# Kernel optimization log

Hardware: AMD Instinct MI355X
Metric: run time of the kernel (lower is better)

## Reference

```python
import jax, jax.numpy as jnp
import numpy as np

B, S, F, H = 2, 2048, 1024, 16
HD = F // H  # head_dim = 64


def rope_embedding(length: int, features: int) -> jnp.ndarray:
    # Faithful copy of the module's unusual RoPE: emb = concat[sin, cos] used as an
    # elementwise multiplier, with symmetric averaging for positions > 0.
    base = 10000.0
    inv_freq = 1.0 / base ** (jnp.arange(0, features, 2, dtype=jnp.float32) / features)
    sinusoid = jnp.einsum('i,j->ij', jnp.arange(length, dtype=jnp.float32), inv_freq)
    sin = jnp.sin(sinusoid)
    cos = jnp.cos(sinusoid)  # features even, so no trailing-column drop
    emb = jnp.concatenate([sin, cos], axis=1)[:, None, :]  # [L, 1, HD]
    if length > 1:
        emb_sym = (emb[1:] + emb[1:][::-1]) / 2.0
        emb = jnp.concatenate([emb[:1], emb_sym], axis=0)
    return emb


def setup_inputs() -> dict:
    key = jax.random.key(0)
    ks = jax.random.split(key, 6)
    scale = 1.0 / np.sqrt(F)
    kv = jax.random.normal(ks[0], (B, S, F), dtype=jnp.float32)
    q = jax.random.normal(ks[1], (B, S, F), dtype=jnp.float32)
    Wq = jax.random.normal(ks[2], (F, F), dtype=jnp.float32) * scale
    Wk = jax.random.normal(ks[3], (F, F), dtype=jnp.float32) * scale
    Wv = jax.random.normal(ks[4], (F, F), dtype=jnp.float32) * scale
    Wo = jax.random.normal(ks[5], (F, F), dtype=jnp.float32) * scale
    mask = jnp.tril(jnp.ones((S, S), dtype=bool))[None, None]  # causal [1,1,S,S]
    return {"kv": kv, "q": q, "Wq": Wq, "Wk": Wk, "Wv": Wv, "Wo": Wo, "mask": mask}


def reference(kv, q, Wq, Wk, Wv, Wo, mask):
    # Dense projections (use_bias=False)
    query = (q @ Wq).reshape(B, S, H, HD)
    key_ = (kv @ Wk).reshape(B, S, H, HD)
    value = (kv @ Wv).reshape(B, S, H, HD)
    # Inline RoPE multiply (module's variant)
    emb = rope_embedding(S, HD)  # [S, 1, HD]
    query = query * emb
    key_ = key_ * emb
    # Scores [B, H, Sq, Sk], scale, mask, softmax
    aw = jnp.einsum('bqhd,bkhd->bhqk', query, key_) / jnp.sqrt(jnp.float32(HD))
    aw = jnp.where(mask, aw, jnp.finfo(jnp.float32).min)
    aw = jax.nn.softmax(aw, axis=-1)
    out = jnp.einsum('bhqk,bkhd->bqhd', aw, value).reshape(B, S, F)
    return out @ Wo
```

## Files before the change

### kernel.cpp

```cpp
#include <hip/hip_runtime.h>

typedef unsigned short u16;
typedef unsigned int u32;

#define S_LEN 2048
#define FEAT 1024
#define NHEAD 16
#define HDIM 64
#define NBATCH 2
#define NROWS (NBATCH * S_LEN)

typedef float f32x4 __attribute__((ext_vector_type(4)));
typedef short s16x8 __attribute__((ext_vector_type(8)));
typedef u32 u32x2 __attribute__((ext_vector_type(2)));

#define LOG2E 1.4426950408889634f

__device__ inline u16 f2bf(float f) {
  u32 u = __float_as_uint(f);
  return (u16)((u + 0x7fffu + ((u >> 16) & 1u)) >> 16);
}

__device__ inline u32 cvt_pk_bf16(float lo, float hi) {
  u32 r;
  asm("v_cvt_pk_bf16_f32 %0, %1, %2" : "=v"(r) : "v"(lo), "v"(hi));
  return r;
}

__device__ inline float fexp2(float x) { return __builtin_amdgcn_exp2f(x); }

__device__ inline f32x4 mfma16(s16x8 a, s16x8 b, f32x4 c) {
  return __builtin_amdgcn_mfma_f32_16x16x32_bf16(a, b, c, 0, 0, 0);
}

typedef __attribute__((address_space(1))) void gvoid;
typedef __attribute__((address_space(3))) void lvoid;
__device__ inline void gload_lds16(const void* g, void* l) {
  __builtin_amdgcn_global_load_lds((gvoid*)g, (lvoid*)l, 16, 0, 0);
}

__device__ inline int swz64(int p) { return p ^ (((p >> 7) & 7) << 4); }

struct us4 { u16 x, y, z, w; };
__global__ __launch_bounds__(256) void prep_kernel(
    const float* __restrict__ q, const float* __restrict__ kv,
    const float* __restrict__ Wq, const float* __restrict__ Wk,
    const float* __restrict__ Wv, const float* __restrict__ Wo,
    u16* __restrict__ qbf, u16* __restrict__ kvbf,
    u16* __restrict__ WqT, u16* __restrict__ WkT,
    u16* __restrict__ WvT, u16* __restrict__ WoT,
    float* __restrict__ emb) {
  __shared__ float tile[32][33];
  int bid = blockIdx.x, tid = threadIdx.x;
  const int n4each = NROWS * FEAT / 4;
  if (bid < 8192) {
    int i = bid * 256 + tid;
    const float* in = q;
    u16* out = qbf;
    if (i >= n4each) { i -= n4each; in = kv; out = kvbf; }
    float4 v = ((const float4*)in)[i];
    us4 o;
    o.x = f2bf(v.x); o.y = f2bf(v.y); o.z = f2bf(v.z); o.w = f2bf(v.w);
    ((us4*)out)[i] = o;
  } else if (bid < 12288) {
    int idx = bid - 8192;
    int z = idx >> 10, rem = idx & 1023;
    int by = rem >> 5, bx = rem & 31;
    const float* W = z == 0 ? Wq : z == 1 ? Wk : z == 2 ? Wv : Wo;
    u16* O = z == 0 ? WqT : z == 1 ? WkT : z == 2 ? WvT : WoT;
    int tx = tid & 31, ty = tid >> 5;
    int bi = bx * 32, bo = by * 32;
#pragma unroll
    for (int r = 0; r < 32; r += 8) tile[ty + r][tx] = W[(bi + ty + r) * FEAT + bo + tx];
    __syncthreads();
#pragma unroll
    for (int r = 0; r < 32; r += 8) O[(bo + ty + r) * FEAT + bi + tx] = f2bf(tile[tx][ty + r]);
  } else {
    int i = (bid - 12288) * 256 + tid;
    if (i >= S_LEN * HDIM) return;
    int p = i >> 6, d = i & 63, j = d & 31;
    float invf = exp2f(-13.287712379549449f * (float)j / 32.0f);
    float a1 = (float)p * invf;
    float v1 = (d < 32) ? sinf(a1) : cosf(a1);
    float e;
    if (p == 0) {
      e = v1;
    } else {
      float a2 = (float)(S_LEN - p) * invf;
      float v2 = (d < 32) ? sinf(a2) : cosf(a2);
      e = 0.5f * (v1 + v2);
    }
    emb[i] = e;
  }
}

__global__ __launch_bounds__(256, 3) void gemm_qkv(
    const u16* __restrict__ qbf, const u16* __restrict__ kvbf,
    const u16* __restrict__ WqT, const u16* __restrict__ WkT, const u16* __restrict__ WvT,
    u16* __restrict__ Qb, u16* __restrict__ Kx, u16* __restrict__ Vx,
    const float* __restrict__ emb) {
  __shared__ __align__(16) u16 lA[3][128 * 32];
  __shared__ __align__(16) u16 lB[3][128 * 32];
  const int K = FEAT;
  int t = threadIdx.x;
  int w = t >> 6, l = t & 63;
  int lr = l & 15, lk = l >> 4;
  int flat = blockIdx.y * 32 + blockIdx.x;
  int xcd = flat & 7, idx = flat >> 3;
  int cx = xcd & 3, cy = xcd >> 2;
  int bx = cx * 8 + (idx & 7);
  int yy = cy * 12 + (idx >> 3);
  int mode = yy >> 3;
  int row0 = bx * 128, col0 = (yy & 7) * 128;
  int wm = w >> 1, wn = w & 1;

  const u16* A = mode == 0 ? qbf : kvbf;
  const u16* Bt = mode == 0 ? WqT : mode == 1 ? WkT : WvT;
  u16* Out = mode == 0 ? Qb : mode == 1 ? Kx : Vx;

  f32x4 acc[4][4] = {};

  int P0 = t * 16, P1 = P0 + 4096;
  int L0 = swz64(P0), L1 = swz64(P1);
  const char* Ab = (const char*)A;
  const char* Bb = (const char*)Bt;
  size_t aOff0 = (size_t)(row0 + (L0 >> 6)) * (K * 2) + (L0 & 63);
  size_t aOff1 = (size_t)(row0 + (L1 >> 6)) * (K * 2) + (L1 & 63);
  size_t bOff0 = (size_t)(col0 + (L0 >> 6)) * (K * 2) + (L0 & 63);
  size_t bOff1 = (size_t)(col0 + (L1 >> 6)) * (K * 2) + (L1 & 63);

  auto stage = [&](int buf, int kt) {
    int kb = kt * 64;
    gload_lds16(Ab + aOff0 + kb, (char*)&lA[buf][0] + w * 1024);
    gload_lds16(Ab + aOff1 + kb, (char*)&lA[buf][0] + w * 1024 + 4096);
    gload_lds16(Bb + bOff0 + kb, (char*)&lB[buf][0] + w * 1024);
    gload_lds16(Bb + bOff1 + kb, (char*)&lB[buf][0] + w * 1024 + 4096);
  };

  stage(0, 0);
  const int NK = K / 32;
  int bufc = 0;
  for (int kt = 0; kt < NK; ++kt) {
    int nb3 = (bufc == 2) ? 0 : bufc + 1;
    if (kt + 1 < NK) {
      stage(nb3, kt + 1);
      asm volatile("s_waitcnt vmcnt(4)" ::: "memory");
    } else {
      asm volatile("s_waitcnt vmcnt(0)" ::: "memory");
    }
    __builtin_amdgcn_s_barrier();

    const char* la = (const char*)&lA[bufc][0];
    const char* lb = (const char*)&lB[bufc][0];
    s16x8 af[4], bfr[4];
#pragma unroll
    for (int mi = 0; mi < 4; ++mi) {
      int byte = (wm * 64 + mi * 16 + lr) * 64 + lk * 16;
      af[mi] = *(const s16x8*)(la + swz64(byte));
    }
#pragma unroll
    for (int ni = 0; ni < 4; ++ni) {
      int byte = (wn * 64 + ni * 16 + lr) * 64 + lk * 16;
      bfr[ni] = *(const s16x8*)(lb + swz64(byte));
    }
    __builtin_amdgcn_s_setprio(1);
#pragma unroll
    for (int mi = 0; mi < 4; ++mi)
#pragma unroll
      for (int ni = 0; ni < 4; ++ni)
        acc[mi][ni] = mfma16(af[mi], bfr[ni], acc[mi][ni]);
    __builtin_amdgcn_s_setprio(0);
    bufc = nb3;
  }

  int rb = row0 + wm * 64 + lk * 4;
  int cb = col0 + wn * 64 + lr;
#pragma unroll
  for (int mi = 0; mi < 4; ++mi)
#pragma unroll
    for (int ni = 0; ni < 4; ++ni) {
      int col = cb + ni * 16;
      int h = col >> 6, d = col & (HDIM - 1);
      if (mode <= 1) {
#pragma unroll
        for (int r = 0; r < 4; ++r) {
          int row = rb + mi * 16 + r;
          int b = row >> 11, s = row & (S_LEN - 1);
          float v = acc[mi][ni][r] * emb[s * HDIM + d];
          if (mode == 0) v *= 0.125f;
          Out[(((b << 4) + h) * S_LEN + s) * HDIM + d] = f2bf(v);
        }
      } else {
        int s0 = rb + mi * 16;
        int b = s0 >> 11, s = s0 & (S_LEN - 1);
        us4 o;
        o.x = f2bf(acc[mi][ni][0]); o.y = f2bf(acc[mi][ni][1]);
        o.z = f2bf(acc[mi][ni][2]); o.w = f2bf(acc[mi][ni][3]);
        *(us4*)&Out[(((b << 4) + h) * HDIM + d) * S_LEN + s] = o;
      }
    }
}

__global__ __launch_bounds__(256, 2) void gemm_oproj(
    const u16* __restrict__ A, const u16* __restrict__ Bt, float* __restrict__ Out) {
  __shared__ __align__(16) u16 lA[3][128 * 32];
  __shared__ __align__(16) u16 lB[3][64 * 32];
  const int K = FEAT, N = FEAT;
  int t = threadIdx.x;
  int w = t >> 6, l = t & 63;
  int lr = l & 15, lk = l >> 4;
  int flat = blockIdx.y * 32 + blockIdx.x;
  int xcd = flat & 7, idx = flat >> 3;
  int cx = xcd & 3, cy = xcd >> 2;
  int bx = cx * 8 + (idx & 7);
  int by = cy * 8 + (idx >> 3);
  int row0 = bx * 128, col0 = by * 64;
  int wm = w >> 1, wn = w & 1;

  f32x4 acc[4][2] = {};

  int P0 = t * 16, P1 = P0 + 4096;
  int L0 = swz64(P0), L1 = swz64(P1);
  const char* Ab = (const char*)A;
  const char* Bb = (const char*)Bt;
  size_t aOff0 = (size_t)(row0 + (L0 >> 6)) * (K * 2) + (L0 & 63);
  size_t aOff1 = (size_t)(row0 + (L1 >> 6)) * (K * 2) + (L1 & 63);
  size_t bOff0 = (size_t)(col0 + (L0 >> 6)) * (K * 2) + (L0 & 63);

  auto stage = [&](int buf, int kt) {
    int kb = kt * 64;
    gload_lds16(Ab + aOff0 + kb, (char*)&lA[buf][0] + w * 1024);
    gload_lds16(Ab + aOff1 + kb, (char*)&lA[buf][0] + w * 1024 + 4096);
    gload_lds16(Bb + bOff0 + kb, (char*)&lB[buf][0] + w * 1024);
  };

  stage(0, 0);
  const int NK = K / 32;
  int bufc = 0;
  for (int kt = 0; kt < NK; ++kt) {
    int nb3 = (bufc == 2) ? 0 : bufc + 1;
    if (kt + 1 < NK) {
      stage(nb3, kt + 1);
      asm volatile("s_waitcnt vmcnt(3)" ::: "memory");
    } else {
      asm volatile("s_waitcnt vmcnt(0)" ::: "memory");
    }
    __builtin_amdgcn_s_barrier();

    const char* la = (const char*)&lA[bufc][0];
    const char* lb = (const char*)&lB[bufc][0];
    s16x8 af[4], bfr[2];
#pragma unroll
    for (int mi = 0; mi < 4; ++mi) {
      int byte = (wm * 64 + mi * 16 + lr) * 64 + lk * 16;
      af[mi] = *(const s16x8*)(la + swz64(byte));
    }
#pragma unroll
    for (int ni = 0; ni < 2; ++ni) {
      int byte = (wn * 32 + ni * 16 + lr) * 64 + lk * 16;
      bfr[ni] = *(const s16x8*)(lb + swz64(byte));
    }
    __builtin_amdgcn_s_setprio(1);
#pragma unroll
    for (int mi = 0; mi < 4; ++mi)
#pragma unroll
      for (int ni = 0; ni < 2; ++ni)
        acc[mi][ni] = mfma16(af[mi], bfr[ni], acc[mi][ni]);
    __builtin_amdgcn_s_setprio(0);
    bufc = nb3;
  }

  int rb = row0 + wm * 64 + lk * 4;
  int cb = col0 + wn * 32 + lr;
#pragma unroll
  for (int mi = 0; mi < 4; ++mi)
#pragma unroll
    for (int ni = 0; ni < 2; ++ni)
#pragma unroll
      for (int r = 0; r < 4; ++r)
        Out[(rb + mi * 16 + r) * N + cb + ni * 16] = acc[mi][ni][r];
}

__global__ __launch_bounds__(256, 2) void attn_kernel(
    const u16* __restrict__ Q, const u16* __restrict__ Kb,
    const u16* __restrict__ Vt, u16* __restrict__ AO) {
  __shared__ __align__(16) u16 lK[3][64 * 64];
  __shared__ __align__(16) u16 lV[3][64 * 64];
  __shared__ __align__(16) u16 lP[4][16 * 64];

  int t = threadIdx.x, w = t >> 6, l = t & 63;
  int lr = l & 15, lk = l >> 4;
  int bid = blockIdx.x;
  int xcd = bid & 7, idx = bid >> 3;
  int bh = xcd * 4 + (idx >> 4), qbp = idx & 15;
  int qtA = qbp, qtB = 31 - qbp;
  int ntA = qtA + 1, ntB = qtB + 1;
  const u16* Qp = Q + bh * (S_LEN * HDIM);
  const char* Kc = (const char*)(Kb + bh * (S_LEN * HDIM));
  const char* Vc = (const char*)(Vt + bh * (HDIM * S_LEN));
  int b = bh >> 4, h = bh & 15;
  int sw = (lr & 7) << 4;

  int P0 = w * 1024 + l * 16;
  int row0 = P0 >> 7;
  int srcK0 = P0 ^ ((row0 & 7) << 4);
  int srcV0 = row0 * 4096 + ((P0 & 127) ^ ((row0 & 7) << 4));

  auto stage = [&](int buf, int kt) {
    gload_lds16(Kc + kt * 8192 + srcK0,          (char*)&lK[buf][0] + w * 1024);
    gload_lds16(Kc + kt * 8192 + srcK0 + 4096,   (char*)&lK[buf][0] + w * 1024 + 4096);
    gload_lds16(Vc + kt * 128 + srcV0,           (char*)&lV[buf][0] + w * 1024);
    gload_lds16(Vc + kt * 128 + srcV0 + 131072,  (char*)&lV[buf][0] + w * 1024 + 4096);
  };

  int qrowA = qtA * 64 + w * 16 + lr;
  int qrowB = qtB * 64 + w * 16 + lr;
  s16x8 qA0 = *(const s16x8*)&Qp[qrowA * HDIM + lk * 8];
  s16x8 qA1 = *(const s16x8*)&Qp[qrowA * HDIM + lk * 8 + 32];
  s16x8 qB0 = *(const s16x8*)&Qp[qrowB * HDIM + lk * 8];
  s16x8 qB1 = *(const s16x8*)&Qp[qrowB * HDIM + lk * 8 + 32];

  f32x4 oA[4] = {}, oB[4] = {};
  float mA = -3.0e38f, lsA = 0.f, mB = -3.0e38f, lsB = 0.f;
  char* plb = (char*)&lP[w][0];

  auto half_sm_pv = [&](f32x4 (&sacc)[4], f32x4 (&oacc)[4], float& m, float& ls,
                        int qrow, bool diag, int kt, const s16x8 (&vf)[4][2]) {
    if (diag) {
#pragma unroll
      for (int nb = 0; nb < 4; ++nb)
#pragma unroll
        for (int r = 0; r < 4; ++r)
          if (kt * 64 + nb * 16 + lk * 4 + r > qrow) sacc[nb][r] = -3.0e38f;
    }
    float tm = sacc[0][0];
#pragma unroll
    for (int nb = 0; nb < 4; ++nb)
#pragma unroll
      for (int r = 0; r < 4; ++r) tm = fmaxf(tm, sacc[nb][r]);
    tm = fmaxf(tm, __shfl_xor(tm, 16, 64));
    tm = fmaxf(tm, __shfl_xor(tm, 32, 64));
    if (!__all(tm <= m + 8.0f)) {
      float mn = fmaxf(m, tm);
      float fs = fexp2((m - mn) * LOG2E);
      m = mn;
      ls *= fs;
#pragma unroll
      for (int nd = 0; nd < 4; ++nd)
#pragma unroll
        for (int r = 0; r < 4; ++r) oacc[nd][r] *= fs;
    }
    float rs = 0.f;
    float p[4][4];
#pragma unroll
    for (int nb = 0; nb < 4; ++nb)
#pragma unroll
      for (int r = 0; r < 4; ++r) {
        float pv = fexp2((sacc[nb][r] - m) * LOG2E);
        p[nb][r] = pv;
        rs += pv;
      }
    rs += __shfl_xor(rs, 16, 64);
    rs += __shfl_xor(rs, 32, 64);
    ls += rs;
#pragma unroll
    for (int nb = 0; nb < 4; ++nb) {
      u32x2 pw;
      pw.x = cvt_pk_bf16(p[nb][0], p[nb][1]);
      pw.y = cvt_pk_bf16(p[nb][2], p[nb][3]);
      int off = (lr * 128 + nb * 32 + lk * 8) ^ sw;
      *(u32x2*)(plb + off) = pw;
    }
    asm volatile("s_waitcnt lgkmcnt(0)" ::: "memory");
    __builtin_amdgcn_sched_barrier(0);
    s16x8 pf0 = *(const s16x8*)(plb + ((lr * 128 + lk * 16) ^ sw));
    s16x8 pf1 = *(const s16x8*)(plb + ((lr * 128 + 64 + lk * 16) ^ sw));
    __builtin_amdgcn_s_setprio(1);
#pragma unroll
    for (int nd = 0; nd < 4; ++nd) {
      oacc[nd] = mfma16(vf[nd][0], pf0, oacc[nd]);
      oacc[nd] = mfma16(vf[nd][1], pf1, oacc[nd]);
    }
    __builtin_amdgcn_s_setprio(0);
  };

  stage(0, 0);
  int bufc = 0;
  const int NT = 33;
  for (int g = 0; g < NT; ++g) {
    int nb3 = (bufc == 2) ? 0 : bufc + 1;
    if (g + 1 < NT) {
      int g1 = g + 1;
      int kt1 = (g1 >= ntA) ? g1 - ntA : g1;
      stage(nb3, kt1);
      asm volatile("s_waitcnt vmcnt(4)" ::: "memory");
    } else {
      asm volatile("s_waitcnt vmcnt(0)" ::: "memory");
    }
    __builtin_amdgcn_s_barrier();

    bool hB = (g >= ntA);
    int kt = hB ? g - ntA : g;
    const char* kb = (const char*)&lK[bufc][0];
    const char* vb = (const char*)&lV[bufc][0];

    s16x8 vf[4][2];
#pragma unroll
    for (int nd = 0; nd < 4; ++nd)
#pragma unroll
      for (int ks = 0; ks < 2; ++ks)
        vf[nd][ks] = *(const s16x8*)(vb + nd * 2048 + lr * 128 + ((lk * 16 + ks * 64) ^ sw));

    s16x8 q0s = hB ? qB0 : qA0;
    s16x8 q1s = hB ? qB1 : qA1;
    f32x4 s4[4] = {};
    __builtin_amdgcn_s_setprio(1);
#pragma unroll
    for (int nb = 0; nb < 4; ++nb)
#pragma unroll
      for (int ks = 0; ks < 2; ++ks) {
        s16x8 kf = *(const s16x8*)(kb + nb * 2048 + lr * 128 + ((lk * 16 + ks * 64) ^ sw));
        s4[nb] = mfma16(kf, ks ? q1s : q0s, s4[nb]);
      }
    __builtin_amdgcn_s_setprio(0);

    if (hB) half_sm_pv(s4, oB, mB, lsB, qrowB, kt == ntB - 1, kt, vf);
    else    half_sm_pv(s4, oA, mA, lsA, qrowA, kt == ntA - 1, kt, vf);

    bufc = nb3;
  }

#pragma unroll
  for (int half = 0; half < 2; ++half) {
    f32x4* oacc = half ? oB : oA;
    float inv = 1.0f / (half ? lsB : lsA);
    int qrow = half ? qrowB : qrowA;
    u16* dst = &AO[(b * S_LEN + qrow) * FEAT + h * HDIM + lk * 4];
#pragma unroll
    for (int nd = 0; nd < 4; ++nd) {
      us4 o;
      o.x = f2bf(oacc[nd][0] * inv);
      o.y = f2bf(oacc[nd][1] * inv);
      o.z = f2bf(oacc[nd][2] * inv);
      o.w = f2bf(oacc[nd][3] * inv);
      *(us4*)(dst + nd * 16) = o;
    }
  }
}

extern "C" void kernel_launch(void* const* d_in, const int* in_sizes, int n_in,
                              void* d_out, int out_size, void* d_ws, size_t ws_size,
                              hipStream_t stream) {
  const float* kv = (const float*)d_in[0];
  const float* q  = (const float*)d_in[1];
  const float* Wq = (const float*)d_in[2];
  const float* Wk = (const float*)d_in[3];
  const float* Wv = (const float*)d_in[4];
  const float* Wo = (const float*)d_in[5];

  float* emb = (float*)d_ws;
  u16* qbf  = (u16*)((char*)d_ws + S_LEN * HDIM * 4);
  u16* kvbf = qbf + NROWS * FEAT;
  u16* WqT  = kvbf + NROWS * FEAT;
  u16* WkT  = WqT + FEAT * FEAT;
  u16* WvT  = WkT + FEAT * FEAT;
  u16* WoT  = WvT + FEAT * FEAT;
  u16* Qb   = WoT + FEAT * FEAT;
  u16* Kx   = Qb + NROWS * FEAT;
  u16* Vx   = Kx + NROWS * FEAT;
  u16* AO   = Vx + NROWS * FEAT;

  prep_kernel<<<12800, 256, 0, stream>>>(q, kv, Wq, Wk, Wv, Wo,
                                         qbf, kvbf, WqT, WkT, WvT, WoT, emb);

  gemm_qkv<<<dim3(NROWS / 128, 24), 256, 0, stream>>>(qbf, kvbf, WqT, WkT, WvT,
                                                      Qb, Kx, Vx, emb);

  attn_kernel<<<512, 256, 0, stream>>>(Qb, Kx, Vx, AO);

  gemm_oproj<<<dim3(NROWS / 128, FEAT / 64), 256, 0, stream>>>(AO, WoT, (float*)d_out);
}
```

Measured before the change: 115.1 us.

## Load V fragments directly from global, deepen K prefetch, defer row-sum reduction

```diff
diff --git a/kernel.cpp b/kernel.cpp
--- a/kernel.cpp
+++ b/kernel.cpp
@@ -284,8 +284,7 @@
 __global__ __launch_bounds__(256, 2) void attn_kernel(
     const u16* __restrict__ Q, const u16* __restrict__ Kb,
     const u16* __restrict__ Vt, u16* __restrict__ AO) {
-  __shared__ __align__(16) u16 lK[3][64 * 64];
-  __shared__ __align__(16) u16 lV[3][64 * 64];
+  __shared__ __align__(16) u16 lK[4][64 * 64];
   __shared__ __align__(16) u16 lP[4][16 * 64];
 
   int t = threadIdx.x, w = t >> 6, l = t & 63;
@@ -297,20 +296,17 @@
   int ntA = qtA + 1, ntB = qtB + 1;
   const u16* Qp = Q + bh * (S_LEN * HDIM);
   const char* Kc = (const char*)(Kb + bh * (S_LEN * HDIM));
-  const char* Vc = (const char*)(Vt + bh * (HDIM * S_LEN));
+  const u16* Vp = Vt + bh * (HDIM * S_LEN);
   int b = bh >> 4, h = bh & 15;
   int sw = (lr & 7) << 4;
 
   int P0 = w * 1024 + l * 16;
   int row0 = P0 >> 7;
   int srcK0 = P0 ^ ((row0 & 7) << 4);
-  int srcV0 = row0 * 4096 + ((P0 & 127) ^ ((row0 & 7) << 4));
-
-  auto stage = [&](int buf, int kt) {
-    gload_lds16(Kc + kt * 8192 + srcK0,          (char*)&lK[buf][0] + w * 1024);
-    gload_lds16(Kc + kt * 8192 + srcK0 + 4096,   (char*)&lK[buf][0] + w * 1024 + 4096);
-    gload_lds16(Vc + kt * 128 + srcV0,           (char*)&lV[buf][0] + w * 1024);
-    gload_lds16(Vc + kt * 128 + srcV0 + 131072,  (char*)&lV[buf][0] + w * 1024 + 4096);
+
+  auto stageK = [&](int buf, int kt) {
+    gload_lds16(Kc + kt * 8192 + srcK0,        (char*)&lK[buf][0] + w * 1024);
+    gload_lds16(Kc + kt * 8192 + srcK0 + 4096, (char*)&lK[buf][0] + w * 1024 + 4096);
   };
 
   int qrowA = qtA * 64 + w * 16 + lr;
@@ -360,8 +356,6 @@
         p[nb][r] = pv;
         rs += pv;
       }
-    rs += __shfl_xor(rs, 16, 64);
-    rs += __shfl_xor(rs, 32, 64);
     ls += rs;
 #pragma unroll
     for (int nb = 0; nb < 4; ++nb) {
@@ -384,16 +378,17 @@
     __builtin_amdgcn_s_setprio(0);
   };
 
-  stage(0, 0);
-  int bufc = 0;
   const int NT = 33;
+  auto ktof = [&](int g) { return (g >= ntA) ? g - ntA : g; };
+
+  stageK(0, ktof(0));
+  stageK(1, ktof(1));
   for (int g = 0; g < NT; ++g) {
-    int nb3 = (bufc == 2) ? 0 : bufc + 1;
-    if (g + 1 < NT) {
-      int g1 = g + 1;
-      int kt1 = (g1 >= ntA) ? g1 - ntA : g1;
-      stage(nb3, kt1);
+    if (g + 2 < NT) {
+      stageK((g + 2) & 3, ktof(g + 2));
       asm volatile("s_waitcnt vmcnt(4)" ::: "memory");
+    } else if (g + 1 < NT) {
+      asm volatile("s_waitcnt vmcnt(2)" ::: "memory");
     } else {
       asm volatile("s_waitcnt vmcnt(0)" ::: "memory");
     }
@@ -401,15 +396,15 @@
 
     bool hB = (g >= ntA);
     int kt = hB ? g - ntA : g;
-    const char* kb = (const char*)&lK[bufc][0];
-    const char* vb = (const char*)&lV[bufc][0];
+    const char* kb = (const char*)&lK[g & 3][0];
 
     s16x8 vf[4][2];
 #pragma unroll
-    for (int nd = 0; nd < 4; ++nd)
-#pragma unroll
-      for (int ks = 0; ks < 2; ++ks)
-        vf[nd][ks] = *(const s16x8*)(vb + nd * 2048 + lr * 128 + ((lk * 16 + ks * 64) ^ sw));
+    for (int nd = 0; nd < 4; ++nd) {
+      const u16* vp = Vp + (nd * 16 + lr) * S_LEN + kt * 64 + lk * 8;
+      vf[nd][0] = *(const s16x8*)vp;
+      vf[nd][1] = *(const s16x8*)(vp + 32);
+    }
 
     s16x8 q0s = hB ? qB0 : qA0;
     s16x8 q1s = hB ? qB1 : qA1;
@@ -426,10 +421,12 @@
 
     if (hB) half_sm_pv(s4, oB, mB, lsB, qrowB, kt == ntB - 1, kt, vf);
     else    half_sm_pv(s4, oA, mA, lsA, qrowA, kt == ntA - 1, kt, vf);
-
-    bufc = nb3;
   }
 
+  lsA += __shfl_xor(lsA, 16, 64);
+  lsA += __shfl_xor(lsA, 32, 64);
+  lsB += __shfl_xor(lsB, 16, 64);
+  lsB += __shfl_xor(lsB, 32, 64);
 #pragma unroll
   for (int half = 0; half < 2; ++half) {
     f32x4* oacc = half ? oB : oA;
```

After: 135.3 us. +17.6%, slower.
